# Kernel tuning notes

Measured on AMD Instinct MI355X. Metric: run time of the kernel, lower is better.

Reference implementation:

```python
import jax, jax.numpy as jnp
import numpy as np

INPUT_DIM, HIDDEN_DIM = 2048, 2048
MEM_SLOTS, MEM_DIM, OUTPUT_DIM = 4096, 1024, 2048


def setup_inputs() -> dict:
    key = jax.random.key(0)
    ks = jax.random.split(key, 16)
    s = 0.02  # small init scale for weights
    return {
        "x": jax.random.normal(ks[0], (1, INPUT_DIM), jnp.float32),
        "h_prev": jax.random.normal(ks[1], (1, HIDDEN_DIM), jnp.float32),
        "c_prev": jax.random.normal(ks[2], (1, HIDDEN_DIM), jnp.float32),
        "memory": jax.random.normal(ks[3], (MEM_SLOTS, MEM_DIM), jnp.float32),
        "usage": jax.random.uniform(ks[4], (MEM_SLOTS,), jnp.float32),
        "read_W": jax.random.normal(ks[5], (MEM_DIM, HIDDEN_DIM), jnp.float32) * s,
        "read_b": jax.random.normal(ks[6], (MEM_DIM,), jnp.float32) * s,
        "W_ih": jax.random.normal(ks[7], (4 * HIDDEN_DIM, INPUT_DIM + MEM_DIM), jnp.float32) * s,
        "b_ih": jax.random.normal(ks[8], (4 * HIDDEN_DIM,), jnp.float32) * s,
        "W_hh": jax.random.normal(ks[9], (4 * HIDDEN_DIM, HIDDEN_DIM), jnp.float32) * s,
        "b_hh": jax.random.normal(ks[10], (4 * HIDDEN_DIM,), jnp.float32) * s,
        "head_W": jax.random.normal(ks[11], (3 * MEM_DIM + MEM_SLOTS + 1, HIDDEN_DIM), jnp.float32) * s,
        "head_b": jax.random.normal(ks[12], (3 * MEM_DIM + MEM_SLOTS + 1,), jnp.float32) * s,
        "out_W": jax.random.normal(ks[13], (OUTPUT_DIM, HIDDEN_DIM + MEM_DIM), jnp.float32) * s,
        "out_b": jax.random.normal(ks[14], (OUTPUT_DIM,), jnp.float32) * s,
    }


def reference(x, h_prev, c_prev, memory, usage,
              read_W, read_b, W_ih, b_ih, W_hh, b_hh,
              head_W, head_b, out_W, out_b):
    M, S = MEM_DIM, MEM_SLOTS
    # --- read ---
    read_key = jnp.tanh(h_prev @ read_W.T + read_b)        # [1, M]
    sim = memory @ read_key[0]                             # [S]
    read_weights = jax.nn.softmax(sim)                     # [S]
    read_vec = read_weights @ memory                       # [M]
    usage_new = usage + read_weights                       # [S]
    # --- LSTM controller (torch LSTMCell gate order: i, f, g, o) ---
    inp = jnp.concatenate([x, read_vec[None, :]], axis=1)  # [1, input+M]
    gates = inp @ W_ih.T + b_ih + h_prev @ W_hh.T + b_hh   # [1, 4H]
    i, f, g, o = jnp.split(gates, 4, axis=1)
    c_new = jax.nn.sigmoid(f) * c_prev + jax.nn.sigmoid(i) * jnp.tanh(g)
    h_new = jax.nn.sigmoid(o) * jnp.tanh(c_new)
    # --- write head params ---
    params = (h_new @ head_W.T + head_b)[0]                # [3M + S + 1]
    erase_vec = jax.nn.sigmoid(params[M:2 * M])            # [M]
    add_vec = jnp.tanh(params[2 * M:3 * M])                # [M]
    w_logits = params[3 * M:3 * M + S]                     # [S]
    write_gate = jax.nn.sigmoid(params[-1])
    w = jax.nn.softmax(w_logits) * write_gate              # [S]
    # slot zeroed if (updated) usage below threshold, then erase/add
    mem_masked = jnp.where(usage_new[:, None] < 0.1, 0.0, memory)
    new_memory = mem_masked * (1.0 - w[:, None] * erase_vec[None, :]) \
                 + w[:, None] * add_vec[None, :]           # [S, M]
    # --- output ---
    out = jnp.concatenate([h_new, read_vec[None, :]], axis=1) @ out_W.T + out_b
    return (out, h_new, c_new, new_memory, usage_new)
```

## Files before the change

### kernel.cpp

```cpp
#include <hip/hip_runtime.h>
#include <math.h>


#define HIDDEN_DIM 2048
#define MEM_SLOTS 4096
#define MEM_DIM 1024

typedef float floatx4 __attribute__((ext_vector_type(4)));

static __device__ __forceinline__ float sigmoidf_(float x) {
    return 1.0f / (1.0f + expf(-x));
}

template<int K4F4>
static __device__ __forceinline__ float rowdot(const float4* __restrict__ Wr,
                                               const float4* __restrict__ v4,
                                               int lane) {
    float a0 = 0.f, a1 = 0.f, a2 = 0.f, a3 = 0.f;
#pragma unroll
    for (int i0 = 0; i0 < K4F4; i0 += 256) {
        int i = i0 + lane;
        floatx4 w0 = *(const floatx4*)(Wr + i);
        floatx4 w1 = *(const floatx4*)(Wr + i + 64);
        floatx4 w2 = *(const floatx4*)(Wr + i + 128);
        floatx4 w3 = *(const floatx4*)(Wr + i + 192);
        floatx4 x0 = *(const floatx4*)(v4 + i);
        floatx4 x1 = *(const floatx4*)(v4 + i + 64);
        floatx4 x2 = *(const floatx4*)(v4 + i + 128);
        floatx4 x3 = *(const floatx4*)(v4 + i + 192);
        a0 = fmaf(w0.x, x0.x, a0); a0 = fmaf(w0.y, x0.y, a0);
        a0 = fmaf(w0.z, x0.z, a0); a0 = fmaf(w0.w, x0.w, a0);
        a1 = fmaf(w1.x, x1.x, a1); a1 = fmaf(w1.y, x1.y, a1);
        a1 = fmaf(w1.z, x1.z, a1); a1 = fmaf(w1.w, x1.w, a1);
        a2 = fmaf(w2.x, x2.x, a2); a2 = fmaf(w2.y, x2.y, a2);
        a2 = fmaf(w2.z, x2.z, a2); a2 = fmaf(w2.w, x2.w, a2);
        a3 = fmaf(w3.x, x3.x, a3); a3 = fmaf(w3.y, x3.y, a3);
        a3 = fmaf(w3.z, x3.z, a3); a3 = fmaf(w3.w, x3.w, a3);
    }
    float acc = (a0 + a1) + (a2 + a3);
#pragma unroll
    for (int off = 32; off > 0; off >>= 1) acc += __shfl_down(acc, off);
    return acc;
}

static __device__ __forceinline__ void do_bg(int u, const float4* whh4,
                                             const float4* wih4, const float4* h4,
                                             const float4* x4, float* gh, float* gx,
                                             int lane) {
    if (u < 8192) {
        float d = rowdot<512>(whh4 + (size_t)u * 512, h4, lane);
        if (lane == 0) gh[u] = d;
    } else {
        int r = u - 8192;
        float d = rowdot<512>(wih4 + (size_t)r * 768, x4, lane);
        if (lane == 0) gx[r] = d;
    }
}

__global__ void k1_rk_bg(const float* __restrict__ read_W, const float* __restrict__ read_b,
                         const float* __restrict__ h_prev, const float* __restrict__ W_hh,
                         const float* __restrict__ W_ih, const float* __restrict__ x,
                         float* __restrict__ rk, float* __restrict__ gh, float* __restrict__ gx) {
    int lane = threadIdx.x & 63;
    int gw = blockIdx.x * 4 + (threadIdx.x >> 6);
    const float4* h4 = (const float4*)h_prev;
    if (gw < 1024) {
        float d = rowdot<512>((const float4*)read_W + (size_t)gw * 512, h4, lane);
        if (lane == 0) rk[gw] = tanhf(d + read_b[gw]);
    } else {
        do_bg(gw - 1024, (const float4*)W_hh, (const float4*)W_ih, h4,
              (const float4*)x, gh, gx, lane);
    }
}

__global__ void k2_sim_bg(const float* __restrict__ memory, const float* __restrict__ rk,
                          const float* __restrict__ h_prev, const float* __restrict__ W_hh,
                          const float* __restrict__ W_ih, const float* __restrict__ x,
                          float* __restrict__ sim, float* __restrict__ gh, float* __restrict__ gx) {
    int lane = threadIdx.x & 63;
    int gw = blockIdx.x * 4 + (threadIdx.x >> 6);
    if (gw < 4096) {
        float d = rowdot<256>((const float4*)memory + (size_t)gw * 256, (const float4*)rk, lane);
        if (lane == 0) sim[gw] = d;
    } else {
        do_bg(3072 + (gw - 4096), (const float4*)W_hh, (const float4*)W_ih,
              (const float4*)h_prev, (const float4*)x, gh, gx, lane);
    }
}

__global__ void k3_smx_bg(const float* __restrict__ sim, const float* __restrict__ usage,
                          float* __restrict__ rw, float* __restrict__ usage_out,
                          const float* __restrict__ h_prev, const float* __restrict__ W_hh,
                          const float* __restrict__ W_ih, const float* __restrict__ x,
                          float* __restrict__ gh, float* __restrict__ gx) {
    int tid = threadIdx.x;
    int lane = tid & 63, wid = tid >> 6;
    if (blockIdx.x != 0) {
        int u = 7168 + (blockIdx.x - 1) * 16 + wid;
        do_bg(u, (const float4*)W_hh, (const float4*)W_ih, (const float4*)h_prev,
              (const float4*)x, gh, gx, lane);
        return;
    }
    __shared__ float sm[16];
    float v0 = sim[tid], v1 = sim[tid + 1024], v2 = sim[tid + 2048], v3 = sim[tid + 3072];
    float m = fmaxf(fmaxf(v0, v1), fmaxf(v2, v3));
#pragma unroll
    for (int off = 32; off > 0; off >>= 1) m = fmaxf(m, __shfl_down(m, off));
    if (lane == 0) sm[wid] = m;
    __syncthreads();
    if (tid == 0) {
        float mm = sm[0];
        for (int i = 1; i < 16; ++i) mm = fmaxf(mm, sm[i]);
        sm[0] = mm;
    }
    __syncthreads();
    float mm = sm[0];
    float e0 = expf(v0 - mm), e1 = expf(v1 - mm), e2 = expf(v2 - mm), e3 = expf(v3 - mm);
    float s = e0 + e1 + e2 + e3;
#pragma unroll
    for (int off = 32; off > 0; off >>= 1) s += __shfl_down(s, off);
    __syncthreads();
    if (lane == 0) sm[wid] = s;
    __syncthreads();
    if (tid == 0) {
        float ss = 0.f;
        for (int i = 0; i < 16; ++i) ss += sm[i];
        sm[0] = ss;
    }
    __syncthreads();
    float inv = 1.f / sm[0];
    float r0 = e0 * inv, r1 = e1 * inv, r2 = e2 * inv, r3 = e3 * inv;
    rw[tid] = r0; rw[tid + 1024] = r1; rw[tid + 2048] = r2; rw[tid + 3072] = r3;
    usage_out[tid]        = usage[tid]        + r0;
    usage_out[tid + 1024] = usage[tid + 1024] + r1;
    usage_out[tid + 2048] = usage[tid + 2048] + r2;
    usage_out[tid + 3072] = usage[tid + 3072] + r3;
}

__global__ void k4_rvp_bg(const float* __restrict__ memory, const float* __restrict__ rw,
                          float* __restrict__ partial,
                          const float* __restrict__ h_prev, const float* __restrict__ W_hh,
                          const float* __restrict__ W_ih, const float* __restrict__ x,
                          float* __restrict__ gh, float* __restrict__ gx) {
    int t = threadIdx.x;
    int lane = t & 63;
    if (blockIdx.x >= 64) {
        int u = 10240 + (blockIdx.x - 64) * 4 + (t >> 6);
        do_bg(u, (const float4*)W_hh, (const float4*)W_ih, (const float4*)h_prev,
              (const float4*)x, gh, gx, lane);
        return;
    }
    int chunk = blockIdx.x;
    const float4* mem4 = (const float4*)memory;
    float4 acc = make_float4(0.f, 0.f, 0.f, 0.f);
    int s0 = chunk * 64;
    for (int s = s0; s < s0 + 64; ++s) {
        float w = rw[s];
        float4 m = mem4[(size_t)s * 256 + t];
        acc.x = fmaf(w, m.x, acc.x);
        acc.y = fmaf(w, m.y, acc.y);
        acc.z = fmaf(w, m.z, acc.z);
        acc.w = fmaf(w, m.w, acc.w);
    }
    ((float4*)partial)[chunk * 256 + t] = acc;
}

__global__ void k5_rvr_bg(const float* __restrict__ partial, float* __restrict__ rv,
                          const float* __restrict__ h_prev, const float* __restrict__ W_hh,
                          const float* __restrict__ W_ih, const float* __restrict__ x,
                          float* __restrict__ gh, float* __restrict__ gx) {
    int tid = threadIdx.x;
    int lane = tid & 63, wid = tid >> 6;
    if (blockIdx.x != 0) {
        int u = 13312 + (blockIdx.x - 1) * 16 + wid;
        do_bg(u, (const float4*)W_hh, (const float4*)W_ih, (const float4*)h_prev,
              (const float4*)x, gh, gx, lane);
        return;
    }
    float s = 0.f;
    for (int k = 0; k < 64; ++k) s += partial[k * 1024 + tid];
    rv[tid] = s;
}

__global__ void k6_grv(const float* __restrict__ W_ih, const float* __restrict__ rv,
                       float* __restrict__ grv) {
    int lane = threadIdx.x & 63;
    int gw = blockIdx.x * 4 + (threadIdx.x >> 6);
    float d = rowdot<256>((const float4*)W_ih + (size_t)gw * 768 + 512, (const float4*)rv, lane);
    if (lane == 0) grv[gw] = d;
}

__global__ void k7_lstm(const float* __restrict__ gx, const float* __restrict__ grv,
                        const float* __restrict__ gh, const float* __restrict__ b_ih,
                        const float* __restrict__ b_hh, const float* __restrict__ c_prev,
                        float* __restrict__ c_new, float* __restrict__ h_new) {
    int t = blockIdx.x * 256 + threadIdx.x;
    float gi = gx[t]        + grv[t]        + gh[t]        + b_ih[t]        + b_hh[t];
    float gf = gx[2048 + t] + grv[2048 + t] + gh[2048 + t] + b_ih[2048 + t] + b_hh[2048 + t];
    float gg = gx[4096 + t] + grv[4096 + t] + gh[4096 + t] + b_ih[4096 + t] + b_hh[4096 + t];
    float go = gx[6144 + t] + grv[6144 + t] + gh[6144 + t] + b_ih[6144 + t] + b_hh[6144 + t];
    float c = sigmoidf_(gf) * c_prev[t] + sigmoidf_(gi) * tanhf(gg);
    float h = sigmoidf_(go) * tanhf(c);
    c_new[t] = c;
    h_new[t] = h;
}

__global__ void k8_head_out(const float* __restrict__ head_W, const float* __restrict__ head_b,
                            const float* __restrict__ out_W, const float* __restrict__ h_new,
                            const float* __restrict__ rv, float* __restrict__ params,
                            float* __restrict__ outh, float* __restrict__ outrv) {
    int lane = threadIdx.x & 63;
    int u = blockIdx.x * 4 + (threadIdx.x >> 6);
    const float4* hn4 = (const float4*)h_new;
    if (u < 6145) {
        int r = 1024 + u;
        float d = rowdot<512>((const float4*)head_W + (size_t)r * 512, hn4, lane);
        if (lane == 0) params[r] = d + head_b[r];
    } else if (u < 8193) {
        int o = u - 6145;
        float d = rowdot<512>((const float4*)out_W + (size_t)o * 768, hn4, lane);
        if (lane == 0) outh[o] = d;
    } else if (u < 10241) {
        int o = u - 8193;
        float d = rowdot<256>((const float4*)out_W + (size_t)o * 768 + 512, (const float4*)rv, lane);
        if (lane == 0) outrv[o] = d;
    }
}

__global__ void k9_smxw(const float* __restrict__ params, float* __restrict__ wv,
                        float* __restrict__ erase, float* __restrict__ addv) {
    __shared__ float sm[16];
    int tid = threadIdx.x;
    int lane = tid & 63, wid = tid >> 6;
    const float* logits = params + 3072;
    float v0 = logits[tid], v1 = logits[tid + 1024], v2 = logits[tid + 2048], v3 = logits[tid + 3072];
    float m = fmaxf(fmaxf(v0, v1), fmaxf(v2, v3));
#pragma unroll
    for (int off = 32; off > 0; off >>= 1) m = fmaxf(m, __shfl_down(m, off));
    if (lane == 0) sm[wid] = m;
    __syncthreads();
    if (tid == 0) {
        float mm = sm[0];
        for (int i = 1; i < 16; ++i) mm = fmaxf(mm, sm[i]);
        sm[0] = mm;
    }
    __syncthreads();
    float mm = sm[0];
    float e0 = expf(v0 - mm), e1 = expf(v1 - mm), e2 = expf(v2 - mm), e3 = expf(v3 - mm);
    float s = e0 + e1 + e2 + e3;
#pragma unroll
    for (int off = 32; off > 0; off >>= 1) s += __shfl_down(s, off);
    __syncthreads();
    if (lane == 0) sm[wid] = s;
    __syncthreads();
    if (tid == 0) {
        float ss = 0.f;
        for (int i = 0; i < 16; ++i) ss += sm[i];
        sm[0] = ss;
    }
    __syncthreads();
    float gate = sigmoidf_(params[7168]);
    float scale = gate / sm[0];
    wv[tid] = e0 * scale; wv[tid + 1024] = e1 * scale;
    wv[tid + 2048] = e2 * scale; wv[tid + 3072] = e3 * scale;
    erase[tid] = sigmoidf_(params[1024 + tid]);
    addv[tid]  = tanhf(params[2048 + tid]);
}

__global__ void k10_memupd(const float* __restrict__ memory, const float* __restrict__ wv,
                           const float* __restrict__ erase, const float* __restrict__ addv,
                           const float* __restrict__ usage_new, float* __restrict__ newmem,
                           const float* __restrict__ outh, const float* __restrict__ outrv,
                           const float* __restrict__ out_b, float* __restrict__ out) {
    int s = blockIdx.x;
    int t = threadIdx.x;
    float w = wv[s];
    float mask = (usage_new[s] < 0.1f) ? 0.f : 1.f;
    float4 m = ((const float4*)memory)[(size_t)s * 256 + t];
    float4 e = ((const float4*)erase)[t];
    float4 a = ((const float4*)addv)[t];
    float4 r;
    r.x = mask * m.x * (1.f - w * e.x) + w * a.x;
    r.y = mask * m.y * (1.f - w * e.y) + w * a.y;
    r.z = mask * m.z * (1.f - w * e.z) + w * a.z;
    r.w = mask * m.w * (1.f - w * e.w) + w * a.w;
    ((float4*)newmem)[(size_t)s * 256 + t] = r;
    if (s < 8) {
        int i = s * 256 + t;
        out[i] = outh[i] + outrv[i] + out_b[i];
    }
}

extern "C" void kernel_launch(void* const* d_in, const int* in_sizes, int n_in,
                              void* d_out_, int out_size, void* d_ws, size_t ws_size,
                              hipStream_t stream) {
    const float* x      = (const float*)d_in[0];
    const float* h_prev = (const float*)d_in[1];
    const float* c_prev = (const float*)d_in[2];
    const float* memory = (const float*)d_in[3];
    const float* usage  = (const float*)d_in[4];
    const float* read_W = (const float*)d_in[5];
    const float* read_b = (const float*)d_in[6];
    const float* W_ih   = (const float*)d_in[7];
    const float* b_ih   = (const float*)d_in[8];
    const float* W_hh   = (const float*)d_in[9];
    const float* b_hh   = (const float*)d_in[10];
    const float* head_W = (const float*)d_in[11];
    const float* head_b = (const float*)d_in[12];
    const float* out_W  = (const float*)d_in[13];
    const float* out_b  = (const float*)d_in[14];

    float* d_out = (float*)d_out_;
    float* ws = (float*)d_ws;

    float* rk      = ws;
    float* sim     = ws + 1024;
    float* rw      = ws + 5120;
    float* rv      = ws + 9216;
    float* gx      = ws + 10240;
    float* gh      = ws + 18432;
    float* grv     = ws + 26624;
    float* params  = ws + 34816;
    float* outh    = ws + 42240;
    float* outrv   = ws + 44288;
    float* wvv     = ws + 46336;
    float* erase   = ws + 50432;
    float* addv    = ws + 51456;
    float* partial = ws + 52480;

    float* out       = d_out;
    float* h_new     = d_out + 2048;
    float* c_new     = d_out + 4096;
    float* newmem    = d_out + 6144;
    float* usage_new = d_out + 6144 + (size_t)MEM_SLOTS * MEM_DIM;

    k1_rk_bg<<<1024, 256, 0, stream>>>(read_W, read_b, h_prev, W_hh, W_ih, x, rk, gh, gx);
    k2_sim_bg<<<2048, 256, 0, stream>>>(memory, rk, h_prev, W_hh, W_ih, x, sim, gh, gx);
    k3_smx_bg<<<193, 1024, 0, stream>>>(sim, usage, rw, usage_new, h_prev, W_hh, W_ih, x, gh, gx);
    k4_rvp_bg<<<832, 256, 0, stream>>>(memory, rw, partial, h_prev, W_hh, W_ih, x, gh, gx);
    k5_rvr_bg<<<193, 1024, 0, stream>>>(partial, rv, h_prev, W_hh, W_ih, x, gh, gx);
    k6_grv<<<2048, 256, 0, stream>>>(W_ih, rv, grv);
    k7_lstm<<<8, 256, 0, stream>>>(gx, grv, gh, b_ih, b_hh, c_prev, c_new, h_new);
    k8_head_out<<<2561, 256, 0, stream>>>(head_W, head_b, out_W, h_new, rv, params, outh, outrv);
    k9_smxw<<<1, 1024, 0, stream>>>(params, wvv, erase, addv);
    k10_memupd<<<4096, 256, 0, stream>>>(memory, wvv, erase, addv, usage_new, newmem,
                                         outh, outrv, out_b, out);
}
```

Baseline: 73.82 us.

## Rebalance background gate GEMV across read-path kernels and move out_W·rv earlier

Redistributes the background W_hh/W_ih·x row-dot work across k1–k5 with new block counts and offsets. k3 and k5 switch to 256-thread blocks, and k5's reduction is vectorised to float4. The out_W·read_vec product moves from k8 into k6, so it runs before the LSTM step and shortens the post-LSTM critical path. This changes how the serial read chain overlaps with the filler work, and it relies on the recomputed unit offsets covering all rows exactly once.

```diff
diff --git a/kernel.cpp b/kernel.cpp
--- a/kernel.cpp
+++ b/kernel.cpp
@@ -62,13 +62,15 @@
                          const float* __restrict__ W_ih, const float* __restrict__ x,
                          float* __restrict__ rk, float* __restrict__ gh, float* __restrict__ gx) {
     int lane = threadIdx.x & 63;
-    int gw = blockIdx.x * 4 + (threadIdx.x >> 6);
+    int wid = threadIdx.x >> 6;
     const float4* h4 = (const float4*)h_prev;
-    if (gw < 1024) {
-        float d = rowdot<512>((const float4*)read_W + (size_t)gw * 512, h4, lane);
-        if (lane == 0) rk[gw] = tanhf(d + read_b[gw]);
+    if (blockIdx.x < 256) {
+        int r = blockIdx.x * 4 + wid;
+        float d = rowdot<512>((const float4*)read_W + (size_t)r * 512, h4, lane);
+        if (lane == 0) rk[r] = tanhf(d + read_b[r]);
     } else {
-        do_bg(gw - 1024, (const float4*)W_hh, (const float4*)W_ih, h4,
+        int u = (blockIdx.x - 256) * 4 + wid;
+        do_bg(u, (const float4*)W_hh, (const float4*)W_ih, h4,
               (const float4*)x, gh, gx, lane);
     }
 }
@@ -78,13 +80,15 @@
                           const float* __restrict__ W_ih, const float* __restrict__ x,
                           float* __restrict__ sim, float* __restrict__ gh, float* __restrict__ gx) {
     int lane = threadIdx.x & 63;
-    int gw = blockIdx.x * 4 + (threadIdx.x >> 6);
-    if (gw < 4096) {
-        float d = rowdot<256>((const float4*)memory + (size_t)gw * 256, (const float4*)rk, lane);
-        if (lane == 0) sim[gw] = d;
+    int wid = threadIdx.x >> 6;
+    if (blockIdx.x < 1024) {
+        int r = blockIdx.x * 4 + wid;
+        float d = rowdot<256>((const float4*)memory + (size_t)r * 256, (const float4*)rk, lane);
+        if (lane == 0) sim[r] = d;
     } else {
-        do_bg(3072 + (gw - 4096), (const float4*)W_hh, (const float4*)W_ih,
-              (const float4*)h_prev, (const float4*)x, gh, gx, lane);
+        int u = 3584 + (blockIdx.x - 1024) * 4 + wid;
+        do_bg(u, (const float4*)W_hh, (const float4*)W_ih, (const float4*)h_prev,
+              (const float4*)x, gh, gx, lane);
     }
 }
 
@@ -96,45 +100,41 @@
     int tid = threadIdx.x;
     int lane = tid & 63, wid = tid >> 6;
     if (blockIdx.x != 0) {
-        int u = 7168 + (blockIdx.x - 1) * 16 + wid;
+        int u = 7680 + (blockIdx.x - 1) * 4 + wid;
         do_bg(u, (const float4*)W_hh, (const float4*)W_ih, (const float4*)h_prev,
               (const float4*)x, gh, gx, lane);
         return;
     }
     __shared__ float sm[16];
-    float v0 = sim[tid], v1 = sim[tid + 1024], v2 = sim[tid + 2048], v3 = sim[tid + 3072];
-    float m = fmaxf(fmaxf(v0, v1), fmaxf(v2, v3));
+    float v[16];
+    float m = -1e30f;
+#pragma unroll
+    for (int j = 0; j < 16; ++j) { v[j] = sim[tid + 256 * j]; m = fmaxf(m, v[j]); }
 #pragma unroll
     for (int off = 32; off > 0; off >>= 1) m = fmaxf(m, __shfl_down(m, off));
     if (lane == 0) sm[wid] = m;
     __syncthreads();
-    if (tid == 0) {
-        float mm = sm[0];
-        for (int i = 1; i < 16; ++i) mm = fmaxf(mm, sm[i]);
-        sm[0] = mm;
-    }
-    __syncthreads();
-    float mm = sm[0];
-    float e0 = expf(v0 - mm), e1 = expf(v1 - mm), e2 = expf(v2 - mm), e3 = expf(v3 - mm);
-    float s = e0 + e1 + e2 + e3;
+    if (tid == 0) sm[8] = fmaxf(fmaxf(sm[0], sm[1]), fmaxf(sm[2], sm[3]));
+    __syncthreads();
+    float mm = sm[8];
+    float e[16], s = 0.f;
+#pragma unroll
+    for (int j = 0; j < 16; ++j) { e[j] = expf(v[j] - mm); s += e[j]; }
 #pragma unroll
     for (int off = 32; off > 0; off >>= 1) s += __shfl_down(s, off);
     __syncthreads();
     if (lane == 0) sm[wid] = s;
     __syncthreads();
-    if (tid == 0) {
-        float ss = 0.f;
-        for (int i = 0; i < 16; ++i) ss += sm[i];
-        sm[0] = ss;
-    }
-    __syncthreads();
-    float inv = 1.f / sm[0];
-    float r0 = e0 * inv, r1 = e1 * inv, r2 = e2 * inv, r3 = e3 * inv;
-    rw[tid] = r0; rw[tid + 1024] = r1; rw[tid + 2048] = r2; rw[tid + 3072] = r3;
-    usage_out[tid]        = usage[tid]        + r0;
-    usage_out[tid + 1024] = usage[tid + 1024] + r1;
-    usage_out[tid + 2048] = usage[tid + 2048] + r2;
-    usage_out[tid + 3072] = usage[tid + 3072] + r3;
+    if (tid == 0) sm[9] = sm[0] + sm[1] + sm[2] + sm[3];
+    __syncthreads();
+    float inv = 1.f / sm[9];
+#pragma unroll
+    for (int j = 0; j < 16; ++j) {
+        int idx = tid + 256 * j;
+        float r = e[j] * inv;
+        rw[idx] = r;
+        usage_out[idx] = usage[idx] + r;
+    }
 }
 
 __global__ void k4_rvp_bg(const float* __restrict__ memory, const float* __restrict__ rw,
@@ -145,7 +145,7 @@
     int t = threadIdx.x;
     int lane = t & 63;
     if (blockIdx.x >= 64) {
-        int u = 10240 + (blockIdx.x - 64) * 4 + (t >> 6);
+        int u = 9728 + (blockIdx.x - 64) * 4 + (t >> 6);
         do_bg(u, (const float4*)W_hh, (const float4*)W_ih, (const float4*)h_prev,
               (const float4*)x, gh, gx, lane);
         return;
@@ -172,22 +172,34 @@
     int tid = threadIdx.x;
     int lane = tid & 63, wid = tid >> 6;
     if (blockIdx.x != 0) {
-        int u = 13312 + (blockIdx.x - 1) * 16 + wid;
+        int u = 14336 + (blockIdx.x - 1) * 4 + wid;
         do_bg(u, (const float4*)W_hh, (const float4*)W_ih, (const float4*)h_prev,
               (const float4*)x, gh, gx, lane);
         return;
     }
-    float s = 0.f;
-    for (int k = 0; k < 64; ++k) s += partial[k * 1024 + tid];
-    rv[tid] = s;
-}
-
-__global__ void k6_grv(const float* __restrict__ W_ih, const float* __restrict__ rv,
-                       float* __restrict__ grv) {
+    const float4* p4 = (const float4*)partial;
+    float4 acc = make_float4(0.f, 0.f, 0.f, 0.f);
+    for (int k = 0; k < 64; ++k) {
+        float4 p = p4[k * 256 + tid];
+        acc.x += p.x; acc.y += p.y; acc.z += p.z; acc.w += p.w;
+    }
+    ((float4*)rv)[tid] = acc;
+}
+
+__global__ void k6_grv_outrv(const float* __restrict__ W_ih, const float* __restrict__ out_W,
+                             const float* __restrict__ rv, float* __restrict__ grv,
+                             float* __restrict__ outrv) {
     int lane = threadIdx.x & 63;
     int gw = blockIdx.x * 4 + (threadIdx.x >> 6);
-    float d = rowdot<256>((const float4*)W_ih + (size_t)gw * 768 + 512, (const float4*)rv, lane);
-    if (lane == 0) grv[gw] = d;
+    const float4* rv4 = (const float4*)rv;
+    if (gw < 8192) {
+        float d = rowdot<256>((const float4*)W_ih + (size_t)gw * 768 + 512, rv4, lane);
+        if (lane == 0) grv[gw] = d;
+    } else {
+        int o = gw - 8192;
+        float d = rowdot<256>((const float4*)out_W + (size_t)o * 768 + 512, rv4, lane);
+        if (lane == 0) outrv[o] = d;
+    }
 }
 
 __global__ void k7_lstm(const float* __restrict__ gx, const float* __restrict__ grv,
@@ -207,8 +219,7 @@
 
 __global__ void k8_head_out(const float* __restrict__ head_W, const float* __restrict__ head_b,
                             const float* __restrict__ out_W, const float* __restrict__ h_new,
-                            const float* __restrict__ rv, float* __restrict__ params,
-                            float* __restrict__ outh, float* __restrict__ outrv) {
+                            float* __restrict__ params, float* __restrict__ outh) {
     int lane = threadIdx.x & 63;
     int u = blockIdx.x * 4 + (threadIdx.x >> 6);
     const float4* hn4 = (const float4*)h_new;
@@ -220,10 +231,6 @@
         int o = u - 6145;
         float d = rowdot<512>((const float4*)out_W + (size_t)o * 768, hn4, lane);
         if (lane == 0) outh[o] = d;
-    } else if (u < 10241) {
-        int o = u - 8193;
-        float d = rowdot<256>((const float4*)out_W + (size_t)o * 768 + 512, (const float4*)rv, lane);
-        if (lane == 0) outrv[o] = d;
     }
 }
 
@@ -334,14 +341,14 @@
     float* newmem    = d_out + 6144;
     float* usage_new = d_out + 6144 + (size_t)MEM_SLOTS * MEM_DIM;
 
-    k1_rk_bg<<<1024, 256, 0, stream>>>(read_W, read_b, h_prev, W_hh, W_ih, x, rk, gh, gx);
+    k1_rk_bg<<<1152, 256, 0, stream>>>(read_W, read_b, h_prev, W_hh, W_ih, x, rk, gh, gx);
     k2_sim_bg<<<2048, 256, 0, stream>>>(memory, rk, h_prev, W_hh, W_ih, x, sim, gh, gx);
-    k3_smx_bg<<<193, 1024, 0, stream>>>(sim, usage, rw, usage_new, h_prev, W_hh, W_ih, x, gh, gx);
-    k4_rvp_bg<<<832, 256, 0, stream>>>(memory, rw, partial, h_prev, W_hh, W_ih, x, gh, gx);
-    k5_rvr_bg<<<193, 1024, 0, stream>>>(partial, rv, h_prev, W_hh, W_ih, x, gh, gx);
-    k6_grv<<<2048, 256, 0, stream>>>(W_ih, rv, grv);
+    k3_smx_bg<<<513, 256, 0, stream>>>(sim, usage, rw, usage_new, h_prev, W_hh, W_ih, x, gh, gx);
+    k4_rvp_bg<<<1216, 256, 0, stream>>>(memory, rw, partial, h_prev, W_hh, W_ih, x, gh, gx);
+    k5_rvr_bg<<<513, 256, 0, stream>>>(partial, rv, h_prev, W_hh, W_ih, x, gh, gx);
+    k6_grv_outrv<<<2560, 256, 0, stream>>>(W_ih, out_W, rv, grv, outrv);
     k7_lstm<<<8, 256, 0, stream>>>(gx, grv, gh, b_ih, b_hh, c_prev, c_new, h_new);
-    k8_head_out<<<2561, 256, 0, stream>>>(head_W, head_b, out_W, h_new, rv, params, outh, outrv);
+    k8_head_out<<<2049, 256, 0, stream>>>(head_W, head_b, out_W, h_new, params, outh);
     k9_smxw<<<1, 1024, 0, stream>>>(params, wvv, erase, addv);
     k10_memupd<<<4096, 256, 0, stream>>>(memory, wvv, erase, addv, usage_new, newmem,
                                          outh, outrv, out_b, out);
```

New measurement: 75.42 us. 1.02x slower.
